# Optimization experiments

Measured on AMD Instinct MI355X. Metric: run time of the kernel, lower is better.

## Reference

```python
import jax, jax.numpy as jnp
import numpy as np

B, N, C = 8, 4096, 768
H, HD = 12, 64          # num_heads, head_dim = C // H
M = HD * 2              # rand_feat_dim
LAM = 0.3
NUM_STEP = 5


def setup_inputs() -> dict:
    key = jax.random.key(0)
    k1, k2, k3, k4 = jax.random.split(key, 4)
    x = jax.random.normal(k1, (B, N, C), dtype=jnp.float32)
    Wqkv = jax.random.normal(k2, (C, 2 * C), dtype=jnp.float32) * 0.02
    Wproj = jax.random.normal(k3, (C, C), dtype=jnp.float32) * 0.02
    bproj = jnp.zeros((C,), dtype=jnp.float32)
    rand_matrix = jax.random.normal(k4, (H, HD, M), dtype=jnp.float32)
    return {"x": x, "Wqkv": Wqkv, "Wproj": Wproj, "bproj": bproj,
            "rand_matrix": rand_matrix}


def _soft(z, t):
    # sign(z) * relu(|z| - t): soft-thresholding (ISTA proximal step)
    return jnp.sign(z) * jax.nn.relu(jnp.abs(z) - t)


def reference(x, Wqkv, Wproj, bproj, rand_matrix):
    Bn, Nn, Cn = x.shape
    Hh, hd, m = rand_matrix.shape
    scale = hd ** (-0.5)

    qkv = x @ Wqkv                                   # [B,N,2C]
    q = qkv[..., :Cn].reshape(Bn, Nn, Hh, hd).transpose(0, 2, 1, 3)  # [B,H,N,hd]
    v = qkv[..., Cn:].reshape(Bn, Nn, Hh, hd).transpose(0, 2, 1, 3)  # [B,H,N,hd]

    # random-feature map: exp(q @ proj - ||q||^2 / 2) / sqrt(m)
    qs = q * scale ** 0.5
    rf = jnp.exp(jnp.einsum('bhnd,hdm->bhnm', qs, rand_matrix)
                 - 0.5 * jnp.sum(qs * qs, axis=-1, keepdims=True)) / m ** 0.5
    # F.normalize(p=2, dim=-2): normalize over the sequence axis
    qn = rf / jnp.maximum(jnp.linalg.norm(rf, axis=-2, keepdims=True), 1e-12)

    kk = jnp.einsum('bhnm,bhnp->bhmp', qn, qn)       # [B,H,m,m]
    kv = jnp.einsum('bhnm,bhnd->bhmd', qn, v)        # [B,H,m,hd]

    # Lipschitz bound: max row L1 norm of kk, detached
    L = jax.lax.stop_gradient(
        jnp.max(jnp.sum(jnp.abs(kk), axis=-1), axis=-1))[..., None, None] + 1.0

    # unrolled ISTA soft-thresholding loop
    s = _soft(kv, LAM)
    for _ in range(NUM_STEP):
        s = _soft(s - (kk @ s - kv) / L, LAM / L)

    out = jnp.einsum('bhnm,bhmd->bhnd', qn, s)       # [B,H,N,hd]
    out = out.transpose(0, 2, 1, 3).reshape(Bn, Nn, Cn)
    return out @ Wproj + bproj
```

## Files before the change

kernel.cpp:

```cpp
#include <hip/hip_runtime.h>


typedef __attribute__((ext_vector_type(8))) short bf16x8;
typedef __attribute__((ext_vector_type(4))) float f32x4;

#define GLD16(gptr, lptr)                                                              \
  __builtin_amdgcn_global_load_lds((const __attribute__((address_space(1))) void*)(gptr), \
                                   (__attribute__((address_space(3))) void*)(lptr), 16, 0, 0)

__device__ __forceinline__ unsigned short f2bf(float f) {
  union { float f; unsigned int u; } v; v.f = f;
  unsigned int r = v.u + 0x7fffu + ((v.u >> 16) & 1u);
  return (unsigned short)(r >> 16);
}
__device__ __forceinline__ float bf2f(unsigned short s) {
  union { unsigned int u; float f; } v; v.u = ((unsigned int)s) << 16;
  return v.f;
}
__device__ __forceinline__ float rn_of(float css) {
  return 1.f / fmaxf(sqrtf(css), 1e-12f);
}

template<int ITERS>
__device__ __forceinline__ void gemm256_core(
    const unsigned short* __restrict__ A,
    const unsigned short* __restrict__ B,
    int ldk,
    f32x4 (&acc)[8][4],
    unsigned short* smem) {
  const int tid = threadIdx.x;
  const int lane = tid & 63, wave = tid >> 6;
  const int l16 = lane & 15, quad = lane >> 4;
  const int wr = wave >> 2, wc = wave & 3;
  const int rsw = l16 & 7;

#pragma unroll
  for (int i = 0; i < 8; i++)
#pragma unroll
    for (int j = 0; j < 4; j++)
#pragma unroll
      for (int r = 0; r < 4; r++) acc[i][j][r] = 0.f;

  const int srow0 = tid >> 3, sc0 = ((tid & 7) ^ (srow0 & 7)) << 3;
  const int srow1 = (tid + 512) >> 3, sc1 = ((tid & 7) ^ (srow1 & 7)) << 3;
  const int dstw = wave * 512;

  auto stageA = [&](int T, int h) {
    const unsigned short* g = A + (long)(h * 128) * ldk + T * 64;
    unsigned short* d = smem + (T & 1) * 32768 + h * 8192 + dstw;
    GLD16(g + (long)srow0 * ldk + sc0, d);
    GLD16(g + (long)srow1 * ldk + sc1, d + 4096);
  };
  auto stageB = [&](int T, int h) {
    const unsigned short* g = B + (long)(h * 128) * ldk + T * 64;
    unsigned short* d = smem + (T & 1) * 32768 + 16384 + h * 8192 + dstw;
    GLD16(g + (long)srow0 * ldk + sc0, d);
    GLD16(g + (long)srow1 * ldk + sc1, d + 4096);
  };

  bf16x8 af[4][2], bn[4][2];

  auto rdA_ks = [&](int b, int mh, int ks) {
    const unsigned short* p = smem + b * 32768 + wr * 8192 + (mh * 64 + l16) * 64;
#pragma unroll
    for (int ii = 0; ii < 4; ii++)
      af[ii][ks] = *(const bf16x8*)(p + ii * 1024 + (((ks * 4 + quad) ^ rsw) << 3));
  };
  auto rdB_ks = [&](int b, int ks) {
    const unsigned short* p = smem + b * 32768 + 16384 + (wc >> 1) * 8192 +
                              ((wc & 1) * 64 + l16) * 64;
#pragma unroll
    for (int jj = 0; jj < 4; jj++)
      bn[jj][ks] = *(const bf16x8*)(p + jj * 1024 + (((ks * 4 + quad) ^ rsw) << 3));
  };

  auto mma16 = [&](int mh, int ks) {
    __builtin_amdgcn_s_setprio(1);
#pragma unroll
    for (int ii = 0; ii < 4; ii++)
#pragma unroll
      for (int jj = 0; jj < 4; jj++)
        acc[mh * 4 + ii][jj] = __builtin_amdgcn_mfma_f32_16x16x32_bf16(
            af[ii][ks], bn[jj][ks], acc[mh * 4 + ii][jj], 0, 0, 0);
    __builtin_amdgcn_s_setprio(0);
  };

#define FENCE asm volatile("" ::: "memory")
#define SGB __builtin_amdgcn_sched_barrier(0)
#define LGKM(n) asm volatile("s_waitcnt lgkmcnt(" #n ")" ::: "memory")

  stageA(0, 0); stageA(0, 1); stageB(0, 0); stageB(0, 1);
  stageB(1, 0); stageB(1, 1);
  asm volatile("s_waitcnt vmcnt(4)" ::: "memory");
  __builtin_amdgcn_s_barrier();

#pragma unroll 1
  for (int i = 0; i < ITERS; i++) {
    const int u = 2 * i;
    const bool more = (i + 1 < ITERS);
    stageA(u + 1, 0);
    rdB_ks(0, 0); rdA_ks(0, 0, 0);
    SGB;
    rdB_ks(0, 1); rdA_ks(0, 0, 1);
    FENCE; __builtin_amdgcn_s_barrier();
    LGKM(8); SGB;
    mma16(0, 0);
    LGKM(0); SGB;
    mma16(0, 1);
    FENCE; __builtin_amdgcn_s_barrier();
    stageA(u + 1, 1);
    if (more) stageB(u + 2, 0);
    rdA_ks(0, 1, 0);
    SGB;
    rdA_ks(0, 1, 1);
    FENCE; __builtin_amdgcn_s_barrier();
    LGKM(4); SGB;
    mma16(1, 0);
    LGKM(0); SGB;
    mma16(1, 1);
    if (more) { asm volatile("s_waitcnt vmcnt(2)" ::: "memory"); }
    else      { asm volatile("s_waitcnt vmcnt(0)" ::: "memory"); }
    FENCE; __builtin_amdgcn_s_barrier();
    if (more) { stageB(u + 2, 1); stageA(u + 2, 0); stageA(u + 2, 1); }
    rdB_ks(1, 0); rdA_ks(1, 0, 0);
    SGB;
    rdB_ks(1, 1); rdA_ks(1, 0, 1);
    FENCE; __builtin_amdgcn_s_barrier();
    LGKM(8); SGB;
    mma16(0, 0);
    LGKM(0); SGB;
    mma16(0, 1);
    FENCE; __builtin_amdgcn_s_barrier();
    if (more) { stageB(u + 3, 0); stageB(u + 3, 1); }
    rdA_ks(1, 1, 0);
    SGB;
    rdA_ks(1, 1, 1);
    FENCE; __builtin_amdgcn_s_barrier();
    LGKM(4); SGB;
    mma16(1, 0);
    LGKM(0); SGB;
    mma16(1, 1);
    if (more) { asm volatile("s_waitcnt vmcnt(4)" ::: "memory"); }
    FENCE; __builtin_amdgcn_s_barrier();
  }
#undef FENCE
#undef SGB
#undef LGKM
}

template<int NT>
__device__ __forceinline__ void gemm128x256_core(
    const unsigned short* __restrict__ A,
    const unsigned short* __restrict__ B,
    int ldk,
    f32x4 (&acc)[4][4],
    unsigned short* smem) {
  const int tid = threadIdx.x;
  const int lane = tid & 63, wave = tid >> 6;
  const int l16 = lane & 15, quad = lane >> 4;
  const int wr = wave >> 2, wc = wave & 3;
  const int rsw = l16 & 7;

#pragma unroll
  for (int m = 0; m < 4; m++)
#pragma unroll
    for (int n = 0; n < 4; n++)
#pragma unroll
      for (int r = 0; r < 4; r++) acc[m][n][r] = 0.f;

  const int srow0 = tid >> 3, sc0 = ((tid & 7) ^ (srow0 & 7)) << 3;
  const int srow1 = (tid + 512) >> 3, sc1 = ((tid & 7) ^ (srow1 & 7)) << 3;
  const int dstw = wave * 512;

  auto stage = [&](int T) {
    unsigned short* d = smem + (T & 1) * 24576;
    const unsigned short* gA = A + T * 64;
    const unsigned short* gB = B + T * 64;
    GLD16(gA + (long)srow0 * ldk + sc0, d + dstw);
    GLD16(gA + (long)srow1 * ldk + sc1, d + 4096 + dstw);
    GLD16(gB + (long)srow0 * ldk + sc0, d + 8192 + dstw);
    GLD16(gB + (long)srow1 * ldk + sc1, d + 8192 + 4096 + dstw);
    GLD16(gB + (long)(srow0 + 128) * ldk + sc0, d + 16384 + dstw);
    GLD16(gB + (long)(srow1 + 128) * ldk + sc1, d + 16384 + 4096 + dstw);
  };

  bf16x8 af[4][2], bn[4][2];

  auto rdA_ks = [&](int b, int ks) {
    const unsigned short* p = smem + b * 24576 + (wr * 64 + l16) * 64;
#pragma unroll
    for (int m = 0; m < 4; m++)
      af[m][ks] = *(const bf16x8*)(p + m * 1024 + (((ks * 4 + quad) ^ rsw) << 3));
  };
  auto rdB_ks = [&](int b, int ks) {
    const unsigned short* p = smem + b * 24576 + 8192 + (wc * 64 + l16) * 64;
#pragma unroll
    for (int n = 0; n < 4; n++)
      bn[n][ks] = *(const bf16x8*)(p + n * 1024 + (((ks * 4 + quad) ^ rsw) << 3));
  };

  auto mma16 = [&](int ks) {
    __builtin_amdgcn_s_setprio(1);
#pragma unroll
    for (int m = 0; m < 4; m++)
#pragma unroll
      for (int n = 0; n < 4; n++)
        acc[m][n] = __builtin_amdgcn_mfma_f32_16x16x32_bf16(
            af[m][ks], bn[n][ks], acc[m][n], 0, 0, 0);
    __builtin_amdgcn_s_setprio(0);
  };

#define FENCE asm volatile("" ::: "memory")
#define SGB __builtin_amdgcn_sched_barrier(0)
#define LGKM(n) asm volatile("s_waitcnt lgkmcnt(" #n ")" ::: "memory")

  stage(0); stage(1);
  asm volatile("s_waitcnt vmcnt(6)" ::: "memory");
  __builtin_amdgcn_s_barrier();

#pragma unroll 1
  for (int t = 0; t < NT; t++) {
    const int b = t & 1;
    rdA_ks(b, 0); rdB_ks(b, 0);
    SGB;
    rdA_ks(b, 1); rdB_ks(b, 1);
    LGKM(8); SGB;
    mma16(0);
    LGKM(0); SGB;
    mma16(1);
    FENCE; __builtin_amdgcn_s_barrier();
    if (t + 2 < NT) stage(t + 2);
    if (t + 1 < NT) {
      if (t + 2 < NT) { asm volatile("s_waitcnt vmcnt(6)" ::: "memory"); }
      else            { asm volatile("s_waitcnt vmcnt(0)" ::: "memory"); }
      FENCE; __builtin_amdgcn_s_barrier();
    }
  }
#undef FENCE
#undef SGB
#undef LGKM
}

__global__ __launch_bounds__(256) void k_pre(const float* __restrict__ x,
                                             unsigned short* __restrict__ xbf,
                                             const float* __restrict__ Wqkv,
                                             unsigned short* __restrict__ wqkvT,
                                             const float* __restrict__ Wproj,
                                             unsigned short* __restrict__ wprojT,
                                             const float* __restrict__ rm,
                                             unsigned short* __restrict__ rmT,
                                             float* __restrict__ colss) {
  __shared__ float t[32][33];
  const int bid = blockIdx.x, tid = threadIdx.x;
  if (bid < 24576) {
    long i = (long)bid * 256 + tid;
    float4 v = ((const float4*)x)[i];
    unsigned short o[4] = {f2bf(v.x), f2bf(v.y), f2bf(v.z), f2bf(v.w)};
    ((uint2*)xbf)[i] = *(uint2*)o;
    return;
  }
  int b2 = bid - 24576;
  const float* in; unsigned short* out; int R, C, c0, r0; float scale;
  if (b2 < 1152) {
    in = Wqkv; out = wqkvT; R = 768; C = 1536;
    c0 = (b2 % 48) * 32; r0 = (b2 / 48) * 32; scale = 1.f;
  } else if (b2 < 1152 + 576) {
    b2 -= 1152;
    in = Wproj; out = wprojT; R = 768; C = 768;
    c0 = (b2 % 24) * 32; r0 = (b2 / 24) * 32; scale = 1.f;
  } else if (b2 < 1152 + 576 + 96) {
    b2 -= 1152 + 576;
    int z = b2 / 8;
    in = rm + (long)z * 8192; out = rmT + (long)z * 8192;
    R = 64; C = 128;
    c0 = (b2 % 4) * 32; r0 = ((b2 / 4) & 1) * 32;
    scale = 0.3535533905932738f;
  } else {
    b2 -= 1152 + 576 + 96;
    colss[b2 * 256 + tid] = 0.f;
    return;
  }
  int tx = tid & 31, ty = tid >> 5;
#pragma unroll
  for (int k = 0; k < 32; k += 8)
    t[ty + k][tx] = in[(long)(r0 + ty + k) * C + c0 + tx];
  __syncthreads();
#pragma unroll
  for (int k = 0; k < 32; k += 8)
    out[(long)(c0 + ty + k) * R + r0 + tx] = f2bf(t[tx][ty + k] * scale);
}

__global__ __launch_bounds__(512, 2) void k_gemm_qkv256(const unsigned short* __restrict__ xbf,
                                                        const unsigned short* __restrict__ wqkvT,
                                                        unsigned short* __restrict__ q,
                                                        unsigned short* __restrict__ vT) {
  __shared__ __align__(16) unsigned short smem[65536];
  f32x4 acc[8][4];
  const int L = blockIdx.x;
  const int xcd = L & 7, slot = L >> 3;
  const int rt = xcd * 16 + slot / 6;
  const int ct = slot % 6;
  gemm256_core<6>(xbf + (long)rt * 256 * 768, wqkvT + (long)ct * 256 * 768, 768, acc, smem);

  const int tid = threadIdx.x, lane = tid & 63, wave = tid >> 6;
  const int l16 = lane & 15, quad = lane >> 4;
  const int wr = wave >> 2, wc = wave & 3;
  const int b = rt >> 4;
  const int nbase = (rt & 15) * 256;
  if (ct < 3) {
#pragma unroll
    for (int i = 0; i < 8; i++)
#pragma unroll
      for (int j = 0; j < 4; j++) {
        int col = ct * 256 + wc * 64 + j * 16 + l16;
        int h = col >> 6, d = col & 63;
#pragma unroll
        for (int r = 0; r < 4; r++) {
          int n = nbase + wr * 128 + i * 16 + quad * 4 + r;
          q[((long)(b * 12 + h) * 4096 + n) * 64 + d] = f2bf(acc[i][j][r]);
        }
      }
  } else {
    unsigned short* pool = smem;
    for (int hh = 0; hh < 2; hh++) {
      __syncthreads();
      if (wr == hh) {
#pragma unroll
        for (int i = 0; i < 8; i++)
#pragma unroll
          for (int j = 0; j < 4; j++)
#pragma unroll
            for (int r = 0; r < 4; r++)
              pool[(wc * 64 + j * 16 + l16) * 136 + i * 16 + quad * 4 + r] = f2bf(acc[i][j][r]);
      }
      __syncthreads();
#pragma unroll
      for (int it = 0; it < 8; it++) {
        int chunk = it * 512 + tid;
        int col = chunk >> 4, ng = chunk & 15;
        uint4 val = *(const uint4*)&pool[col * 136 + ng * 8];
        int vcol = (ct - 3) * 256 + col;
        int h = vcol >> 6, d = vcol & 63;
        long n = nbase + hh * 128 + ng * 8;
        *(uint4*)&vT[((long)(b * 12 + h) * 64 + d) * 4096 + n] = val;
      }
    }
  }
}

__global__ __launch_bounds__(256) void k_gemm_rf(const unsigned short* __restrict__ q,
                                                 const unsigned short* __restrict__ rmT,
                                                 unsigned short* __restrict__ qnT,
                                                 float* __restrict__ colss) {
  __shared__ __align__(16) unsigned short smem[16384];
  __shared__ float hnp[256];
  __shared__ float css[128];
  unsigned short* Asm = smem;
  unsigned short* Bsm = smem + 8192;
  unsigned short* pool = smem;
  f32x4 acc[4][4];
  const int nt = blockIdx.x, bh = blockIdx.y, h = bh % 12;
  const int tid = threadIdx.x, lane = tid & 63, wave = tid >> 6;
  const int l16 = lane & 15, quad = lane >> 4;
  const int wm = (wave >> 1) * 64, wn = (wave & 1) * 64;
  const int fsw = (l16 >> 1) & 3;
  const unsigned short* Aq = q + ((long)bh * 4096 + nt * 128) * 64;
  const unsigned short* Brm = rmT + (long)h * 8192;

#pragma unroll
  for (int c = 0; c < 4; c++) {
    int chunk = c * 256 + tid;
    int row = chunk >> 3, ko8 = chunk & 7;
    int kc = ko8 >> 2;
    int c2s = (ko8 & 3) ^ ((row >> 1) & 3);
    *(uint4*)(Asm + kc * 4096 + row * 32 + c2s * 8) = *(const uint4*)(Aq + (long)row * 64 + ko8 * 8);
    *(uint4*)(Bsm + kc * 4096 + row * 32 + c2s * 8) = *(const uint4*)(Brm + (long)row * 64 + ko8 * 8);
  }
  for (int i = tid; i < 128; i += 256) css[i] = 0.f;
  __syncthreads();
  {
    const unsigned short* ap = Asm + (tid & 1) * 4096 + (tid >> 1) * 32;
    float ssum = 0.f;
#pragma unroll
    for (int e = 0; e < 32; e++) { float f = bf2f(ap[e]); ssum += f * f; }
    hnp[tid] = ssum;
  }
#pragma unroll
  for (int i = 0; i < 4; i++)
#pragma unroll
    for (int j = 0; j < 4; j++)
#pragma unroll
      for (int r = 0; r < 4; r++) acc[i][j][r] = 0.f;
#pragma unroll
  for (int kc = 0; kc < 2; kc++) {
    bf16x8 af[4], bfr[4];
#pragma unroll
    for (int i = 0; i < 4; i++)
      af[i] = *(const bf16x8*)(Asm + kc * 4096 + (wm + i * 16 + l16) * 32 + ((quad ^ fsw) * 8));
#pragma unroll
    for (int j = 0; j < 4; j++)
      bfr[j] = *(const bf16x8*)(Bsm + kc * 4096 + (wn + j * 16 + l16) * 32 + ((quad ^ fsw) * 8));
#pragma unroll
    for (int i = 0; i < 4; i++)
#pragma unroll
      for (int j = 0; j < 4; j++)
        acc[i][j] = __builtin_amdgcn_mfma_f32_16x16x32_bf16(af[i], bfr[j], acc[i][j], 0, 0, 0);
  }
  __syncthreads();
  float hnv[4][4];
#pragma unroll
  for (int i = 0; i < 4; i++)
#pragma unroll
    for (int r = 0; r < 4; r++) {
      int row = wm + i * 16 + quad * 4 + r;
      hnv[i][r] = 0.0625f * (hnp[2 * row] + hnp[2 * row + 1]);
    }
#pragma unroll
  for (int j = 0; j < 4; j++) {
    int col = wn + j * 16 + l16;
    float cp = 0.f;
#pragma unroll
    for (int i = 0; i < 4; i++)
#pragma unroll
      for (int r = 0; r < 4; r++) {
        float v = __expf(acc[i][j][r] - hnv[i][r]) * 0.08838834764831845f;
        acc[i][j][r] = v;
        cp += v * v;
      }
    atomicAdd(&css[col], cp);
  }
  __syncthreads();
  for (int i = tid; i < 128; i += 256) atomicAdd(&colss[bh * 128 + i], css[i]);
  for (int hh = 0; hh < 2; hh++) {
    __syncthreads();
    if ((wave >> 1) == hh) {
#pragma unroll
      for (int i = 0; i < 4; i++)
#pragma unroll
        for (int j = 0; j < 4; j++)
#pragma unroll
          for (int r = 0; r < 4; r++)
            pool[(i * 16 + quad * 4 + r) * 134 + wn + j * 16 + l16] = f2bf(acc[i][j][r]);
    }
    __syncthreads();
#pragma unroll
    for (int c = 0; c < 4; c++) {
      int chunk = tid + c * 256;
      int m = chunk >> 3, nj = (chunk & 7) * 8;
      unsigned short o[8];
#pragma unroll
      for (int e = 0; e < 8; e++) o[e] = pool[(nj + e) * 134 + m];
      *(uint4*)&qnT[((long)bh * 128 + m) * 4096 + nt * 128 + hh * 64 + nj] = *(uint4*)o;
    }
  }
}

__global__ __launch_bounds__(256) void k_gemm_kkkv(const unsigned short* __restrict__ qnT,
                                                   const unsigned short* __restrict__ vT,
                                                   const float* __restrict__ colss,
                                                   unsigned short* __restrict__ kkp) {
  __shared__ __align__(16) unsigned short sm[12288];
  f32x4 acc[4][6];
  const int ks = blockIdx.x, bh = blockIdx.y;
  const unsigned short* A = qnT + (long)bh * 128 * 4096 + ks * 512;
  const unsigned short* B1 = vT + (long)bh * 64 * 4096 + ks * 512;
  const int tid = threadIdx.x, lane = tid & 63, wave = tid >> 6;
  const int l16 = lane & 15, quad = lane >> 4;
  const int wm = (wave >> 1) * 64, wn = (wave & 1) * 96;
  const int arow = tid >> 2;
  const int akos = (((tid & 3) ^ ((arow >> 1) & 3)) << 3);
  const int fsw = (l16 >> 1) & 3;
#pragma unroll
  for (int i = 0; i < 4; i++)
#pragma unroll
    for (int j = 0; j < 6; j++)
#pragma unroll
      for (int r = 0; r < 4; r++) acc[i][j][r] = 0.f;

  auto stage = [&](int t) {
    unsigned short* d = sm + (t & 1) * 6144;
    GLD16(A + (long)arow * 4096 + t * 32 + akos, d + wave * 512);
    GLD16(A + (long)(arow + 64) * 4096 + t * 32 + akos, d + 2048 + wave * 512);
    GLD16(B1 + (long)arow * 4096 + t * 32 + akos, d + 4096 + wave * 512);
  };

  stage(0); stage(1);
  asm volatile("s_waitcnt vmcnt(3)" ::: "memory");
  __builtin_amdgcn_s_barrier();

#pragma unroll 1
  for (int t = 0; t < 16; t++) {
    const unsigned short* As = sm + (t & 1) * 6144;
    const unsigned short* Bs = As + 4096;
    bf16x8 af[4], bfr[6];
#pragma unroll
    for (int i = 0; i < 4; i++)
      af[i] = *(const bf16x8*)(As + (wm + i * 16 + l16) * 32 + ((quad ^ fsw) * 8));
#pragma unroll
    for (int j = 0; j < 6; j++) {
      int row = wn + j * 16 + l16;
      const unsigned short* rp = (row < 128) ? (As + row * 32) : (Bs + (row - 128) * 32);
      bfr[j] = *(const bf16x8*)(rp + ((quad ^ fsw) * 8));
    }
    asm volatile("s_waitcnt lgkmcnt(0)" ::: "memory");
    __builtin_amdgcn_sched_barrier(0);
    __builtin_amdgcn_s_setprio(1);
#pragma unroll
    for (int i = 0; i < 4; i++)
#pragma unroll
      for (int j = 0; j < 6; j++)
        acc[i][j] = __builtin_amdgcn_mfma_f32_16x16x32_bf16(af[i], bfr[j], acc[i][j], 0, 0, 0);
    __builtin_amdgcn_s_setprio(0);
    asm volatile("" ::: "memory");
    __builtin_amdgcn_s_barrier();
    if (t + 2 < 16) stage(t + 2);
    if (t + 1 < 16) {
      if (t + 2 < 16) { asm volatile("s_waitcnt vmcnt(3)" ::: "memory"); }
      else            { asm volatile("s_waitcnt vmcnt(0)" ::: "memory"); }
      asm volatile("" ::: "memory");
      __builtin_amdgcn_s_barrier();
    }
  }

  unsigned short* dst = kkp + ((long)ks * 96 + bh) * 24576;
  float rnr[4][4];
#pragma unroll
  for (int i = 0; i < 4; i++)
#pragma unroll
    for (int r = 0; r < 4; r++)
      rnr[i][r] = rn_of(colss[bh * 128 + wm + i * 16 + quad * 4 + r]);
#pragma unroll
  for (int j = 0; j < 6; j++) {
    int col = wn + j * 16 + l16;
    float rnc = (col < 128) ? rn_of(colss[bh * 128 + col]) : 1.f;
#pragma unroll
    for (int i = 0; i < 4; i++)
#pragma unroll
      for (int r = 0; r < 4; r++) {
        int row = wm + i * 16 + quad * 4 + r;
        dst[row * 192 + col] = f2bf(acc[i][j][r] * rnr[i][r] * rnc);
      }
  }
}

__global__ __launch_bounds__(256) void k_red(const unsigned short* __restrict__ kkp,
                                             unsigned short* __restrict__ kkred,
                                             float* __restrict__ kvred) {
  const int g = blockIdx.x, bh = blockIdx.y;
  const int tid = threadIdx.x;
  const unsigned short* base = kkp + (long)bh * 24576 + (long)(g * 32) * 192;
#pragma unroll
  for (int c = 0; c < 3; c++) {
    int idx = c * 256 + tid;
    int m = idx / 24, c8 = idx % 24;
    float f[8] = {0.f, 0.f, 0.f, 0.f, 0.f, 0.f, 0.f, 0.f};
#pragma unroll
    for (int ks = 0; ks < 8; ks++) {
      union { uint4 u; unsigned short s[8]; } u;
      u.u = *(const uint4*)(base + (long)ks * 2359296 + m * 192 + c8 * 8);
#pragma unroll
      for (int e = 0; e < 8; e++) f[e] += bf2f(u.s[e]);
    }
    long row = (long)bh * 128 + g * 32 + m;
    if (c8 < 16) {
      unsigned short o[8];
#pragma unroll
      for (int e = 0; e < 8; e++) o[e] = f2bf(f[e]);
      *(uint4*)&kkred[row * 128 + c8 * 8] = *(uint4*)o;
    } else {
      *(float4*)&kvred[row * 64 + (c8 - 16) * 8] = make_float4(f[0], f[1], f[2], f[3]);
      *(float4*)&kvred[row * 64 + (c8 - 16) * 8 + 4] = make_float4(f[4], f[5], f[6], f[7]);
    }
  }
}

__global__ __launch_bounds__(256) void k_ista2(const unsigned short* __restrict__ kkred,
                                               const float* __restrict__ kvred,
                                               const float* __restrict__ colss,
                                               unsigned short* __restrict__ sT) {
  __shared__ __align__(16) unsigned short kks[128 * 144];
  __shared__ __align__(16) unsigned short ssT[32 * 144];
  __shared__ float kvs[128 * 32];
  __shared__ float red[128];
  __shared__ float rns[128];
  const int tid = threadIdx.x, lane = tid & 63, wave = tid >> 6;
  const int l16 = lane & 15, quad = lane >> 4;
  const int wm = (wave >> 1) * 64, wn = (wave & 1) * 16;
  const int bh = blockIdx.x >> 1, d0 = (blockIdx.x & 1) * 32;
  for (int idx = tid; idx < 2048; idx += 256) {
    int m = idx >> 4, c8 = idx & 15;
    uint4 v = *(const uint4*)(kkred + ((long)bh * 128 + m) * 128 + c8 * 8);
    *(uint4*)&kks[m * 144 + c8 * 8] = v;
  }
  for (int idx = tid; idx < 1024; idx += 256) {
    int m = idx >> 3, c4 = idx & 7;
    float4 v = *(const float4*)(kvred + ((long)bh * 128 + m) * 64 + d0 + c4 * 4);
    *(float4*)&kvs[m * 32 + c4 * 4] = v;
  }
  __syncthreads();
  float kv[4][4];
#pragma unroll
  for (int i = 0; i < 4; i++)
#pragma unroll
    for (int r = 0; r < 4; r++) {
      int m = wm + i * 16 + quad * 4 + r, dl = wn + l16;
      kv[i][r] = kvs[m * 32 + dl];
    }
  if (tid < 128) {
    float rs = 0.f;
    const unsigned short* rp = kks + tid * 144;
    for (int p = 0; p < 128; p++) rs += fabsf(bf2f(rp[p]));
    red[tid] = rs;
    rns[tid] = rn_of(colss[bh * 128 + tid]);
  }
  __syncthreads();
  for (int o = 64; o > 0; o >>= 1) {
    if (tid < o) red[tid] = fmaxf(red[tid], red[tid + o]);
    __syncthreads();
  }
  const float L = red[0] + 1.f;
  const float invL = 1.f / L;
  const float lamL = 0.3f * invL;
  float sreg[4][4];
#pragma unroll
  for (int i = 0; i < 4; i++)
#pragma unroll
    for (int r = 0; r < 4; r++) {
      float z = kv[i][r];
      float az = fabsf(z) - 0.3f;
      float s = az > 0.f ? copysignf(az, z) : 0.f;
      sreg[i][r] = s;
      ssT[(wn + l16) * 144 + wm + i * 16 + quad * 4 + r] = f2bf(s);
    }
  for (int step = 0; step < 5; step++) {
    __syncthreads();
    f32x4 acc[4];
#pragma unroll
    for (int i = 0; i < 4; i++)
#pragma unroll
      for (int r = 0; r < 4; r++) acc[i][r] = 0.f;
#pragma unroll
    for (int kc = 0; kc < 4; kc++) {
      bf16x8 af[4], bfj;
#pragma unroll
      for (int i = 0; i < 4; i++)
        af[i] = *(const bf16x8*)(kks + (wm + i * 16 + l16) * 144 + kc * 32 + quad * 8);
      bfj = *(const bf16x8*)(ssT + (wn + l16) * 144 + kc * 32 + quad * 8);
#pragma unroll
      for (int i = 0; i < 4; i++)
        acc[i] = __builtin_amdgcn_mfma_f32_16x16x32_bf16(af[i], bfj, acc[i], 0, 0, 0);
    }
    __syncthreads();
#pragma unroll
    for (int i = 0; i < 4; i++)
#pragma unroll
      for (int r = 0; r < 4; r++) {
        float z = sreg[i][r] - (acc[i][r] - kv[i][r]) * invL;
        float az = fabsf(z) - lamL;
        float s = az > 0.f ? copysignf(az, z) : 0.f;
        sreg[i][r] = s;
        ssT[(wn + l16) * 144 + wm + i * 16 + quad * 4 + r] = f2bf(s);
      }
  }
#pragma unroll
  for (int i = 0; i < 4; i++)
#pragma unroll
    for (int r = 0; r < 4; r++) {
      int m = wm + i * 16 + quad * 4 + r, d = d0 + wn + l16;
      sT[(long)bh * 8192 + d * 128 + m] = f2bf(sreg[i][r] * rns[m]);
    }
}

__global__ __launch_bounds__(256) void k_gemm_attn(const unsigned short* __restrict__ qnT,
                                                   const unsigned short* __restrict__ sT,
                                                   unsigned short* __restrict__ attn) {
  __shared__ __align__(16) unsigned short As2[17408];
  __shared__ __align__(16) unsigned short Bs[8192];
  f32x4 acc[4][2];
  const int nt = blockIdx.x, bh = blockIdx.y;
  const int b = bh / 12, h = bh % 12;
  const int tid = threadIdx.x, lane = tid & 63, wave = tid >> 6;
  const int l16 = lane & 15, quad = lane >> 4;
  const int wm = (wave >> 1) * 64, wn = (wave & 1) * 32;
  const int fsw = (l16 >> 1) & 3;
#pragma unroll
  for (int i = 0; i < 4; i++)
#pragma unroll
    for (int j = 0; j < 2; j++)
#pragma unroll
      for (int r = 0; r < 4; r++) acc[i][j][r] = 0.f;

#pragma unroll
  for (int it = 0; it < 9; it++) {
    if (it < 8 || tid < 128) {
      int c = it * 256 + tid;
      int rt_ = (c * 241) >> 12;
      int nh = c - rt_ * 17;
      int kc = rt_ >> 5, p = rt_ & 31;
      int k = kc * 32 + ((p & 7) << 2) + (p >> 3);
      int n8 = (nh < 16 ? nh : 15) << 3;
      const unsigned short* gp = qnT + ((long)bh * 128 + k) * 4096 + nt * 128 + n8;
      GLD16(gp, As2 + c * 8);
    }
  }
#pragma unroll
  for (int it = 0; it < 4; it++) {
    int c = it * 256 + tid;
    int kcp = c >> 8, c8 = c & 255;
    int dd = c8 >> 2, sub = c8 & 3;
    int ko = kcp * 32 + ((sub ^ ((dd >> 1) & 3)) << 3);
    const unsigned short* gp = sT + ((long)bh * 64 + dd) * 128 + ko;
    GLD16(gp, Bs + c * 8);
  }
  asm volatile("s_waitcnt vmcnt(0)" ::: "memory");
  __builtin_amdgcn_s_barrier();

#pragma unroll
  for (int kc = 0; kc < 4; kc++) {
    bf16x8 af[4], bfr[2];
#pragma unroll
    for (int i = 0; i < 4; i++) {
      union { bf16x8 v; unsigned short s[8]; } u;
#pragma unroll
      for (int e = 0; e < 8; e++) {
        int p = ((e & 3) << 3) + (quad << 1) + (e >> 2);
        u.s[e] = As2[(kc * 32 + p) * 136 + wm + i * 16 + l16];
      }
      af[i] = u.v;
    }
#pragma unroll
    for (int j = 0; j < 2; j++)
      bfr[j] = *(const bf16x8*)&Bs[kc * 2048 + (wn + j * 16 + l16) * 32 + ((quad ^ fsw) * 8)];
#pragma unroll
    for (int i = 0; i < 4; i++)
#pragma unroll
      for (int j = 0; j < 2; j++)
        acc[i][j] = __builtin_amdgcn_mfma_f32_16x16x32_bf16(af[i], bfr[j], acc[i][j], 0, 0, 0);
  }
#pragma unroll
  for (int i = 0; i < 4; i++)
#pragma unroll
    for (int j = 0; j < 2; j++)
#pragma unroll
      for (int r = 0; r < 4; r++) {
        int n = nt * 128 + wm + i * 16 + quad * 4 + r;
        int dd = wn + j * 16 + l16;
        attn[((long)b * 4096 + n) * 768 + h * 64 + dd] = f2bf(acc[i][j][r]);
      }
}

__global__ __launch_bounds__(512, 2) void k_gemm_proj128(const unsigned short* __restrict__ attn,
                                                         const unsigned short* __restrict__ wprojT,
                                                         const float* __restrict__ bias,
                                                         float* __restrict__ out) {
  __shared__ __align__(16) unsigned short smem[49152];
  f32x4 acc[4][4];
  const int L = blockIdx.x;
  const int xcd = L & 7, slot = L >> 3;
  const int rt = xcd * 32 + slot / 3;
  const int ct = slot % 3;
  gemm128x256_core<12>(attn + (long)rt * 128 * 768, wprojT + (long)ct * 256 * 768, 768,
                       acc, smem);
  const int tid = threadIdx.x, lane = tid & 63, wave = tid >> 6;
  const int l16 = lane & 15, quad = lane >> 4;
  const int wr = wave >> 2, wc = wave & 3;
  const long row0 = (long)rt * 128 + wr * 64;
#pragma unroll
  for (int m = 0; m < 4; m++)
#pragma unroll
    for (int n = 0; n < 4; n++) {
      int col = ct * 256 + wc * 64 + n * 16 + l16;
      float bv = bias[col];
#pragma unroll
      for (int r = 0; r < 4; r++) {
        long row = row0 + m * 16 + quad * 4 + r;
        out[row * 768 + col] = acc[m][n][r] + bv;
      }
    }
}

extern "C" void kernel_launch(void* const* d_in, const int* in_sizes, int n_in,
                              void* d_out, int out_size, void* d_ws, size_t ws_size,
                              hipStream_t stream) {
  const float* x = (const float*)d_in[0];
  const float* Wqkv = (const float*)d_in[1];
  const float* Wproj = (const float*)d_in[2];
  const float* bproj = (const float*)d_in[3];
  const float* rm = (const float*)d_in[4];
  float* out = (float*)d_out;

  size_t o = 0;
  char* wsb = (char*)d_ws;
  auto take = [&](size_t b) { char* p = wsb + o; o += b; return p; };
  unsigned short* wqkvT = (unsigned short*)take(2359296);
  unsigned short* wprojT = (unsigned short*)take(1179648);
  unsigned short* rmT = (unsigned short*)take(196608);
  unsigned short* q = (unsigned short*)take(50331648);
  unsigned short* vT = (unsigned short*)take(50331648);
  float* colss = (float*)take(49152);
  unsigned short* sT = (unsigned short*)take(1572864);
  if (ws_size < o) return;

  unsigned short* xbf = (unsigned short*)d_out;
  unsigned short* qnT = (unsigned short*)d_out;
  unsigned short* kkp = q;
  unsigned short* attnbf = q;
  unsigned short* kkred = vT;
  float* kvred = (float*)(vT + 1572864);

  k_pre<<<26448, 256, 0, stream>>>(x, xbf, Wqkv, wqkvT, Wproj, wprojT, rm, rmT, colss);
  k_gemm_qkv256<<<768, 512, 0, stream>>>(xbf, wqkvT, q, vT);
  k_gemm_rf<<<dim3(32, 96), 256, 0, stream>>>(q, rmT, qnT, colss);
  k_gemm_kkkv<<<dim3(8, 96), 256, 0, stream>>>(qnT, vT, colss, kkp);
  k_red<<<dim3(4, 96), 256, 0, stream>>>(kkp, kkred, kvred);
  k_ista2<<<192, 256, 0, stream>>>(kkred, kvred, colss, sT);
  k_gemm_attn<<<dim3(32, 96), 256, 0, stream>>>(qnT, sT, attnbf);
  k_gemm_proj128<<<768, 512, 0, stream>>>(attnbf, wprojT, bproj, out);
}
```

Measured before the change: 442.3 us.

## Persistent double-buffered rf kernel, vectorized ISTA row sums, register-transpose attn loads

```diff
diff --git a/kernel.cpp b/kernel.cpp
--- a/kernel.cpp
+++ b/kernel.cpp
@@ -352,19 +352,17 @@
                                                  const unsigned short* __restrict__ rmT,
                                                  unsigned short* __restrict__ qnT,
                                                  float* __restrict__ colss) {
-  __shared__ __align__(16) unsigned short smem[16384];
+  __shared__ __align__(16) unsigned short smem[33152];
   __shared__ float hnp[256];
   __shared__ float css[128];
-  unsigned short* Asm = smem;
-  unsigned short* Bsm = smem + 8192;
-  unsigned short* pool = smem;
+  unsigned short* Bsm = smem + 16384;
+  unsigned short* pool = smem + 24576;
   f32x4 acc[4][4];
-  const int nt = blockIdx.x, bh = blockIdx.y, h = bh % 12;
+  const int nt4 = blockIdx.x, bh = blockIdx.y, h = bh % 12;
   const int tid = threadIdx.x, lane = tid & 63, wave = tid >> 6;
   const int l16 = lane & 15, quad = lane >> 4;
   const int wm = (wave >> 1) * 64, wn = (wave & 1) * 64;
   const int fsw = (l16 >> 1) & 3;
-  const unsigned short* Aq = q + ((long)bh * 4096 + nt * 128) * 64;
   const unsigned short* Brm = rmT + (long)h * 8192;
 
 #pragma unroll
@@ -373,86 +371,114 @@
     int row = chunk >> 3, ko8 = chunk & 7;
     int kc = ko8 >> 2;
     int c2s = (ko8 & 3) ^ ((row >> 1) & 3);
-    *(uint4*)(Asm + kc * 4096 + row * 32 + c2s * 8) = *(const uint4*)(Aq + (long)row * 64 + ko8 * 8);
+    const unsigned short* Aq0 = q + ((long)bh * 4096 + nt4 * 512) * 64;
+    *(uint4*)(smem + kc * 4096 + row * 32 + c2s * 8) = *(const uint4*)(Aq0 + (long)row * 64 + ko8 * 8);
     *(uint4*)(Bsm + kc * 4096 + row * 32 + c2s * 8) = *(const uint4*)(Brm + (long)row * 64 + ko8 * 8);
   }
   for (int i = tid; i < 128; i += 256) css[i] = 0.f;
   __syncthreads();
-  {
-    const unsigned short* ap = Asm + (tid & 1) * 4096 + (tid >> 1) * 32;
-    float ssum = 0.f;
-#pragma unroll
-    for (int e = 0; e < 32; e++) { float f = bf2f(ap[e]); ssum += f * f; }
-    hnp[tid] = ssum;
-  }
-#pragma unroll
-  for (int i = 0; i < 4; i++)
-#pragma unroll
-    for (int j = 0; j < 4; j++)
-#pragma unroll
-      for (int r = 0; r < 4; r++) acc[i][j][r] = 0.f;
-#pragma unroll
-  for (int kc = 0; kc < 2; kc++) {
-    bf16x8 af[4], bfr[4];
+
+#pragma unroll 1
+  for (int st = 0; st < 4; st++) {
+    const int buf = st & 1;
+    const int nt = nt4 * 4 + st;
+    uint4 avreg[4];
+    if (st < 3) {
+      const unsigned short* Aq = q + ((long)bh * 4096 + (nt + 1) * 128) * 64;
+#pragma unroll
+      for (int c = 0; c < 4; c++) {
+        int chunk = c * 256 + tid;
+        int row = chunk >> 3, ko8 = chunk & 7;
+        avreg[c] = *(const uint4*)(Aq + (long)row * 64 + ko8 * 8);
+      }
+    }
+    {
+      const unsigned short* ap = smem + buf * 8192 + (tid & 1) * 4096 + (tid >> 1) * 32;
+      float ssum = 0.f;
+#pragma unroll
+      for (int e = 0; e < 32; e++) { float f = bf2f(ap[e]); ssum += f * f; }
+      hnp[tid] = ssum;
+    }
 #pragma unroll
     for (int i = 0; i < 4; i++)
-      af[i] = *(const bf16x8*)(Asm + kc * 4096 + (wm + i * 16 + l16) * 32 + ((quad ^ fsw) * 8));
-#pragma unroll
-    for (int j = 0; j < 4; j++)
-      bfr[j] = *(const bf16x8*)(Bsm + kc * 4096 + (wn + j * 16 + l16) * 32 + ((quad ^ fsw) * 8));
+#pragma unroll
+      for (int j = 0; j < 4; j++)
+#pragma unroll
+        for (int r = 0; r < 4; r++) acc[i][j][r] = 0.f;
+#pragma unroll
+    for (int kc = 0; kc < 2; kc++) {
+      bf16x8 af[4], bfr[4];
+#pragma unroll
+      for (int i = 0; i < 4; i++)
+        af[i] = *(const bf16x8*)(smem + buf * 8192 + kc * 4096 + (wm + i * 16 + l16) * 32 +
+                                 ((quad ^ fsw) * 8));
+#pragma unroll
+      for (int j = 0; j < 4; j++)
+        bfr[j] = *(const bf16x8*)(Bsm + kc * 4096 + (wn + j * 16 + l16) * 32 + ((quad ^ fsw) * 8));
+#pragma unroll
+      for (int i = 0; i < 4; i++)
+#pragma unroll
+        for (int j = 0; j < 4; j++)
+          acc[i][j] = __builtin_amdgcn_mfma_f32_16x16x32_bf16(af[i], bfr[j], acc[i][j], 0, 0, 0);
+    }
+    __syncthreads();
+    float hnv[4][4];
 #pragma unroll
     for (int i = 0; i < 4; i++)
 #pragma unroll
-      for (int j = 0; j < 4; j++)
-        acc[i][j] = __builtin_amdgcn_mfma_f32_16x16x32_bf16(af[i], bfr[j], acc[i][j], 0, 0, 0);
-  }
-  __syncthreads();
-  float hnv[4][4];
-#pragma unroll
-  for (int i = 0; i < 4; i++)
-#pragma unroll
-    for (int r = 0; r < 4; r++) {
-      int row = wm + i * 16 + quad * 4 + r;
-      hnv[i][r] = 0.0625f * (hnp[2 * row] + hnp[2 * row + 1]);
-    }
-#pragma unroll
-  for (int j = 0; j < 4; j++) {
-    int col = wn + j * 16 + l16;
-    float cp = 0.f;
-#pragma unroll
-    for (int i = 0; i < 4; i++)
-#pragma unroll
       for (int r = 0; r < 4; r++) {
-        float v = __expf(acc[i][j][r] - hnv[i][r]) * 0.08838834764831845f;
-        acc[i][j][r] = v;
-        cp += v * v;
-      }
-    atomicAdd(&css[col], cp);
-  }
-  __syncthreads();
+        int row = wm + i * 16 + quad * 4 + r;
+        hnv[i][r] = 0.0625f * (hnp[2 * row] + hnp[2 * row + 1]);
+      }
+#pragma unroll
+    for (int j = 0; j < 4; j++) {
+      int col = wn + j * 16 + l16;
+      float cp = 0.f;
+#pragma unroll
+      for (int i = 0; i < 4; i++)
+#pragma unroll
+        for (int r = 0; r < 4; r++) {
+          float v = __expf(acc[i][j][r] - hnv[i][r]) * 0.08838834764831845f;
+          acc[i][j][r] = v;
+          cp += v * v;
+        }
+      atomicAdd(&css[col], cp);
+    }
+    for (int hh = 0; hh < 2; hh++) {
+      __syncthreads();
+      if ((wave >> 1) == hh) {
+#pragma unroll
+        for (int i = 0; i < 4; i++)
+#pragma unroll
+          for (int j = 0; j < 4; j++)
+#pragma unroll
+            for (int r = 0; r < 4; r++)
+              pool[(i * 16 + quad * 4 + r) * 134 + wn + j * 16 + l16] = f2bf(acc[i][j][r]);
+      }
+      __syncthreads();
+#pragma unroll
+      for (int c = 0; c < 4; c++) {
+        int chunk = tid + c * 256;
+        int m = chunk >> 3, nj = (chunk & 7) * 8;
+        unsigned short o[8];
+#pragma unroll
+        for (int e = 0; e < 8; e++) o[e] = pool[(nj + e) * 134 + m];
+        *(uint4*)&qnT[((long)bh * 128 + m) * 4096 + nt * 128 + hh * 64 + nj] = *(uint4*)o;
+      }
+    }
+    if (st < 3) {
+#pragma unroll
+      for (int c = 0; c < 4; c++) {
+        int chunk = c * 256 + tid;
+        int row = chunk >> 3, ko8 = chunk & 7;
+        int kc2 = ko8 >> 2;
+        int c2s = (ko8 & 3) ^ ((row >> 1) & 3);
+        *(uint4*)(smem + (buf ^ 1) * 8192 + kc2 * 4096 + row * 32 + c2s * 8) = avreg[c];
+      }
+    }
+    __syncthreads();
+  }
   for (int i = tid; i < 128; i += 256) atomicAdd(&colss[bh * 128 + i], css[i]);
-  for (int hh = 0; hh < 2; hh++) {
-    __syncthreads();
-    if ((wave >> 1) == hh) {
-#pragma unroll
-      for (int i = 0; i < 4; i++)
-#pragma unroll
-        for (int j = 0; j < 4; j++)
-#pragma unroll
-          for (int r = 0; r < 4; r++)
-            pool[(i * 16 + quad * 4 + r) * 134 + wn + j * 16 + l16] = f2bf(acc[i][j][r]);
-    }
-    __syncthreads();
-#pragma unroll
-    for (int c = 0; c < 4; c++) {
-      int chunk = tid + c * 256;
-      int m = chunk >> 3, nj = (chunk & 7) * 8;
-      unsigned short o[8];
-#pragma unroll
-      for (int e = 0; e < 8; e++) o[e] = pool[(nj + e) * 134 + m];
-      *(uint4*)&qnT[((long)bh * 128 + m) * 4096 + nt * 128 + hh * 64 + nj] = *(uint4*)o;
-    }
-  }
 }
 
 __global__ __launch_bounds__(256) void k_gemm_kkkv(const unsigned short* __restrict__ qnT,
@@ -582,6 +608,7 @@
   __shared__ __align__(16) unsigned short ssT[32 * 144];
   __shared__ float kvs[128 * 32];
   __shared__ float red[128];
+  __shared__ float redp[256];
   __shared__ float rns[128];
   const int tid = threadIdx.x, lane = tid & 63, wave = tid >> 6;
   const int l16 = lane & 15, quad = lane >> 4;
@@ -606,13 +633,21 @@
       int m = wm + i * 16 + quad * 4 + r, dl = wn + l16;
       kv[i][r] = kvs[m * 32 + dl];
     }
-  if (tid < 128) {
+  {
+    const unsigned short* rp = kks + (tid >> 1) * 144 + (tid & 1) * 64;
     float rs = 0.f;
-    const unsigned short* rp = kks + tid * 144;
-    for (int p = 0; p < 128; p++) rs += fabsf(bf2f(rp[p]));
-    red[tid] = rs;
-    rns[tid] = rn_of(colss[bh * 128 + tid]);
-  }
+#pragma unroll
+    for (int c = 0; c < 8; c++) {
+      union { uint4 u; unsigned short s[8]; } u;
+      u.u = *(const uint4*)(rp + c * 8);
+#pragma unroll
+      for (int e = 0; e < 8; e++) rs += fabsf(bf2f(u.s[e]));
+    }
+    redp[tid] = rs;
+  }
+  if (tid < 128) rns[tid] = rn_of(colss[bh * 128 + tid]);
+  __syncthreads();
+  if (tid < 128) red[tid] = redp[2 * tid] + redp[2 * tid + 1];
   __syncthreads();
   for (int o = 64; o > 0; o >>= 1) {
     if (tid < o) red[tid] = fmaxf(red[tid], red[tid + o]);
@@ -690,19 +725,12 @@
 #pragma unroll
       for (int r = 0; r < 4; r++) acc[i][j][r] = 0.f;
 
-#pragma unroll
-  for (int it = 0; it < 9; it++) {
-    if (it < 8 || tid < 128) {
-      int c = it * 256 + tid;
-      int rt_ = (c * 241) >> 12;
-      int nh = c - rt_ * 17;
-      int kc = rt_ >> 5, p = rt_ & 31;
-      int k = kc * 32 + ((p & 7) << 2) + (p >> 3);
-      int n8 = (nh < 16 ? nh : 15) << 3;
-      const unsigned short* gp = qnT + ((long)bh * 128 + k) * 4096 + nt * 128 + n8;
-      GLD16(gp, As2 + c * 8);
-    }
-  }
+  const int m8 = tid >> 4, n8 = tid & 15;
+  union U8 { uint4 v; unsigned short s[8]; };
+  U8 in8[8], outp[8];
+#pragma unroll
+  for (int e = 0; e < 8; e++)
+    in8[e].v = *(const uint4*)(qnT + ((long)bh * 128 + m8 * 8 + e) * 4096 + nt * 128 + n8 * 8);
 #pragma unroll
   for (int it = 0; it < 4; it++) {
     int c = it * 256 + tid;
@@ -712,21 +740,26 @@
     const unsigned short* gp = sT + ((long)bh * 64 + dd) * 128 + ko;
     GLD16(gp, Bs + c * 8);
   }
-  asm volatile("s_waitcnt vmcnt(0)" ::: "memory");
-  __builtin_amdgcn_s_barrier();
+#pragma unroll
+  for (int j = 0; j < 8; j++)
+#pragma unroll
+    for (int e = 0; e < 8; e++) outp[j].s[e] = in8[e].s[j];
+  {
+    int swz = m8 ^ (n8 & 7);
+#pragma unroll
+    for (int j = 0; j < 8; j++)
+      *(uint4*)(As2 + (n8 * 8 + j) * 136 + swz * 8) = outp[j].v;
+  }
+  __syncthreads();
 
 #pragma unroll
   for (int kc = 0; kc < 4; kc++) {
     bf16x8 af[4], bfr[2];
 #pragma unroll
     for (int i = 0; i < 4; i++) {
-      union { bf16x8 v; unsigned short s[8]; } u;
-#pragma unroll
-      for (int e = 0; e < 8; e++) {
-        int p = ((e & 3) << 3) + (quad << 1) + (e >> 2);
-        u.s[e] = As2[(kc * 32 + p) * 136 + wm + i * 16 + l16];
-      }
-      af[i] = u.v;
+      int n = wm + i * 16 + l16;
+      int phys = (kc * 4 + quad) ^ ((n >> 3) & 7);
+      af[i] = *(const bf16x8*)(As2 + n * 136 + phys * 8);
     }
 #pragma unroll
     for (int j = 0; j < 2; j++)
@@ -810,7 +843,7 @@
 
   k_pre<<<26448, 256, 0, stream>>>(x, xbf, Wqkv, wqkvT, Wproj, wprojT, rm, rmT, colss);
   k_gemm_qkv256<<<768, 512, 0, stream>>>(xbf, wqkvT, q, vT);
-  k_gemm_rf<<<dim3(32, 96), 256, 0, stream>>>(q, rmT, qnT, colss);
+  k_gemm_rf<<<dim3(8, 96), 256, 0, stream>>>(q, rmT, qnT, colss);
   k_gemm_kkkv<<<dim3(8, 96), 256, 0, stream>>>(qnT, vT, colss, kkp);
   k_red<<<dim3(4, 96), 256, 0, stream>>>(kkp, kkred, kvred);
   k_ista2<<<192, 256, 0, stream>>>(kkred, kvred, colss, sT);
```

After: 456.0 us. 3.1% more time.
